# Optimization experiments

Measured on AMD Instinct MI355X. Metric: run time of the kernel, lower is better.

The kernel has to match this reference:

```python
import jax, jax.numpy as jnp
import numpy as np

N, E = 50000, 800000
IN_CH, HID, OUT, EDIM = 151, 128, 51, 51


def setup_inputs() -> dict:
    key = jax.random.key(0)
    ks = jax.random.split(key, 10)
    def w(k, shape, fan_in):
        return jax.random.normal(k, shape, jnp.float32) * (1.0 / np.sqrt(fan_in))
    return {
        "x": jax.random.normal(ks[0], (N, IN_CH), jnp.float32),
        "edge_attr": jax.random.normal(ks[1], (E, EDIM), jnp.float32),
        "W_edge0": w(ks[2], (EDIM, IN_CH), EDIM),
        "b_edge0": jnp.zeros((IN_CH,), jnp.float32),
        "W0": w(ks[3], (IN_CH, HID), IN_CH),
        "b0": jnp.zeros((HID,), jnp.float32),
        "W_edge1": w(ks[4], (EDIM, HID), EDIM),
        "b_edge1": jnp.zeros((HID,), jnp.float32),
        "W1": w(ks[5], (HID, HID), HID),
        "b1": jnp.zeros((HID,), jnp.float32),
        "W_out": w(ks[6], (HID, OUT), HID),
        "b_out": jnp.zeros((OUT,), jnp.float32),
        "edge_index": jax.random.randint(ks[7], (2, E), 0, N, jnp.int32),
    }


def gtn_layer(x, src, dst, edge_attr, W_e, b_e, W, b):
    # message: x_j + Linear(edge_attr);  aggr='add' scatter to dst.
    eat = edge_attr @ W_e + b_e                                # [E, in_ch]
    msgs = x[src] + eat                                        # gather + add
    agg = jax.ops.segment_sum(msgs, dst, num_segments=x.shape[0])
    # self-loops carry zero edge_attr -> transformed attr == bias b_e,
    # so their message is x + b_e (equivalent to concatenating N self-loop edges).
    agg = agg + x + b_e
    return agg @ W + b                                         # self.linear


def reference(x, edge_attr, W_edge0, b_edge0, W0, b0, W_edge1, b_edge1, W1, b1, W_out, b_out, edge_index):
    src, dst = edge_index[0], edge_index[1]
    h = gtn_layer(x, src, dst, edge_attr, W_edge0, b_edge0, W0, b0)   # [N, HID]
    h = gtn_layer(h, src, dst, edge_attr, W_edge1, b_edge1, W1, b1)   # [N, HID]
    # global_mean_pool with batch=arange(N) is identity (one node per graph)
    return h @ W_out + b_out                                          # [N, OUT]
```

## Files before the change

### kernel.cpp

```cpp
#include <hip/hip_runtime.h>

#define N_NODES 50000
#define N_EDGES 800000
#define IN_CH   151
#define HID     128
#define OUT_CH  51
#define EDIM    51
#define WP      64
#define LSTR    68
#define NBLK    ((N_NODES + 255) / 256)

static __device__ __forceinline__ unsigned int f2bf(float f) {
    union { float f; unsigned int u; } v; v.f = f;
    unsigned int r = v.u + 0x7FFF + ((v.u >> 16) & 1);
    return r >> 16;
}
static __device__ __forceinline__ float bflo(unsigned int u) {
    return __uint_as_float(u << 16);
}
static __device__ __forceinline__ float bfhi(unsigned int u) {
    return __uint_as_float(u & 0xFFFF0000u);
}

__global__ void kw1(const float* __restrict__ We0, const float* __restrict__ W0,
                    const float* __restrict__ be0, const float* __restrict__ W1,
                    const float* __restrict__ Wout,
                    float* __restrict__ M0, float* __restrict__ c0, float* __restrict__ Wc) {
    int t = blockIdx.x * blockDim.x + threadIdx.x;
    if (t < 51 * 128) {
        int i = t / 128, j = t % 128;
        float a = 0.f;
        for (int k = 0; k < IN_CH; ++k) a += We0[i * IN_CH + k] * W0[k * HID + j];
        M0[t] = a;
    } else if (t < 51 * 128 + 128) {
        int j = t - 51 * 128;
        float a = 0.f;
        for (int k = 0; k < IN_CH; ++k) a += be0[k] * W0[k * HID + j];
        c0[j] = a;
    } else if (t < 51 * 128 + 128 + 128 * WP) {
        int u = t - (51 * 128 + 128);
        int i = u / WP, j = u % WP;
        float a = 0.f;
        if (j < OUT_CH)
            for (int k = 0; k < HID; ++k) a += W1[i * HID + k] * Wout[k * OUT_CH + j];
        Wc[i * WP + j] = a;
    }
}

__global__ void kw2(const float* __restrict__ We1, const float* __restrict__ be1,
                    const float* __restrict__ b1, const float* __restrict__ Wout,
                    const float* __restrict__ bout, const float* __restrict__ Wc,
                    float* __restrict__ Mc, float* __restrict__ cc, float* __restrict__ dd) {
    int t = blockIdx.x * blockDim.x + threadIdx.x;
    if (t < 51 * WP) {
        int i = t / WP, j = t % WP;
        float a = 0.f;
        if (j < OUT_CH)
            for (int k = 0; k < HID; ++k) a += We1[i * HID + k] * Wc[k * WP + j];
        Mc[t] = a;
    } else if (t < 51 * WP + 51) {
        int j = t - 51 * WP;
        float a = 0.f;
        for (int k = 0; k < HID; ++k) a += be1[k] * Wc[k * WP + j];
        cc[j] = a;
    } else if (t < 51 * WP + 102) {
        int j = t - (51 * WP + 51);
        float a = 0.f;
        for (int k = 0; k < HID; ++k) a += b1[k] * Wout[k * OUT_CH + j];
        dd[j] = a + bout[j];
    }
}

__global__ void k_hist(const int* __restrict__ ei, int* __restrict__ deg) {
    int e = blockIdx.x * 256 + threadIdx.x;
    if (e >= N_EDGES) return;
    atomicAdd(&deg[ei[N_EDGES + e]], 1);
}

__global__ void scan1(const int* __restrict__ deg, int* __restrict__ blksum) {
    __shared__ int lds[256];
    int i = blockIdx.x * 256 + threadIdx.x;
    lds[threadIdx.x] = (i < N_NODES) ? deg[i] : 0;
    __syncthreads();
    for (int s = 128; s > 0; s >>= 1) {
        if (threadIdx.x < s) lds[threadIdx.x] += lds[threadIdx.x + s];
        __syncthreads();
    }
    if (threadIdx.x == 0) blksum[blockIdx.x] = lds[0];
}

__global__ void scan2(const int* __restrict__ blksum, int* __restrict__ blkoff) {
    __shared__ int lds[256];
    int v = (threadIdx.x < NBLK) ? blksum[threadIdx.x] : 0;
    lds[threadIdx.x] = v;
    __syncthreads();
    for (int s = 1; s < 256; s <<= 1) {
        int t = (threadIdx.x >= s) ? lds[threadIdx.x - s] : 0;
        __syncthreads();
        lds[threadIdx.x] += t;
        __syncthreads();
    }
    if (threadIdx.x < NBLK) blkoff[threadIdx.x] = lds[threadIdx.x] - v;
}

__global__ void scan3(const int* __restrict__ deg, const int* __restrict__ blkoff,
                      int* __restrict__ row_start, int* __restrict__ cursor) {
    __shared__ int lds[256];
    int i = blockIdx.x * 256 + threadIdx.x;
    int v = (i < N_NODES) ? deg[i] : 0;
    lds[threadIdx.x] = v;
    __syncthreads();
    for (int s = 1; s < 256; s <<= 1) {
        int t = (threadIdx.x >= s) ? lds[threadIdx.x - s] : 0;
        __syncthreads();
        lds[threadIdx.x] += t;
        __syncthreads();
    }
    if (i < N_NODES) {
        int ex = blkoff[blockIdx.x] + lds[threadIdx.x] - v;
        row_start[i] = ex;
        cursor[i] = ex;
    }
    if (blockIdx.x == 0 && threadIdx.x == 0) row_start[N_NODES] = N_EDGES;
}

__global__ void k_fill(const int* __restrict__ ei, int* __restrict__ cursor,
                       int* __restrict__ eid_sorted, int* __restrict__ src_sorted) {
    int e = blockIdx.x * 256 + threadIdx.x;
    if (e >= N_EDGES) return;
    int dst = ei[N_EDGES + e];
    int pos = atomicAdd(&cursor[dst], 1);
    eid_sorted[pos] = e;
    src_sorted[pos] = ei[e];
}

__global__ void k_agg_S(const float* __restrict__ ea, const int* __restrict__ eid_sorted,
                        const int* __restrict__ row_start, float* __restrict__ S) {
    int n = blockIdx.x * 4 + (threadIdx.x >> 6);
    if (n >= N_NODES) return;
    int lane = threadIdx.x & 63;
    int n0 = row_start[n], n1 = row_start[n + 1];
    float acc = 0.f;
    bool act = lane < EDIM;
    for (int base = n0; base < n1; base += 64) {
        int cnt = min(64, n1 - base);
        int eid_l = (base + lane < n1) ? eid_sorted[base + lane] : 0;
        int t = 0;
        for (; t + 8 <= cnt; t += 8) {
            int e0 = __shfl(eid_l, t),     e1 = __shfl(eid_l, t + 1);
            int e2 = __shfl(eid_l, t + 2), e3 = __shfl(eid_l, t + 3);
            int e4 = __shfl(eid_l, t + 4), e5 = __shfl(eid_l, t + 5);
            int e6 = __shfl(eid_l, t + 6), e7 = __shfl(eid_l, t + 7);
            float v0 = act ? ea[(size_t)e0 * EDIM + lane] : 0.f;
            float v1 = act ? ea[(size_t)e1 * EDIM + lane] : 0.f;
            float v2 = act ? ea[(size_t)e2 * EDIM + lane] : 0.f;
            float v3 = act ? ea[(size_t)e3 * EDIM + lane] : 0.f;
            float v4 = act ? ea[(size_t)e4 * EDIM + lane] : 0.f;
            float v5 = act ? ea[(size_t)e5 * EDIM + lane] : 0.f;
            float v6 = act ? ea[(size_t)e6 * EDIM + lane] : 0.f;
            float v7 = act ? ea[(size_t)e7 * EDIM + lane] : 0.f;
            acc += ((v0 + v1) + (v2 + v3)) + ((v4 + v5) + (v6 + v7));
        }
        for (; t < cnt; ++t) {
            int e0 = __shfl(eid_l, t);
            if (act) acc += ea[(size_t)e0 * EDIM + lane];
        }
    }
    if (act) S[(size_t)n * EDIM + lane] = acc;
}

__global__ void k_agg_h(const unsigned int* __restrict__ yb, const int* __restrict__ src_sorted,
                        const int* __restrict__ row_start, float* __restrict__ hacc) {
    int n = blockIdx.x * 4 + (threadIdx.x >> 6);
    if (n >= N_NODES) return;
    int lane = threadIdx.x & 63;
    int n0 = row_start[n], n1 = row_start[n + 1];
    float2 acc = make_float2(0.f, 0.f);
    for (int base = n0; base < n1; base += 64) {
        int cnt = min(64, n1 - base);
        int s_l = (base + lane < n1) ? src_sorted[base + lane] : 0;
        int t = 0;
        for (; t + 8 <= cnt; t += 8) {
            int s0 = __shfl(s_l, t),     s1 = __shfl(s_l, t + 1);
            int s2 = __shfl(s_l, t + 2), s3 = __shfl(s_l, t + 3);
            int s4 = __shfl(s_l, t + 4), s5 = __shfl(s_l, t + 5);
            int s6 = __shfl(s_l, t + 6), s7 = __shfl(s_l, t + 7);
            unsigned int v0 = yb[(size_t)s0 * 64 + lane];
            unsigned int v1 = yb[(size_t)s1 * 64 + lane];
            unsigned int v2 = yb[(size_t)s2 * 64 + lane];
            unsigned int v3 = yb[(size_t)s3 * 64 + lane];
            unsigned int v4 = yb[(size_t)s4 * 64 + lane];
            unsigned int v5 = yb[(size_t)s5 * 64 + lane];
            unsigned int v6 = yb[(size_t)s6 * 64 + lane];
            unsigned int v7 = yb[(size_t)s7 * 64 + lane];
            acc.x += ((bflo(v0) + bflo(v1)) + (bflo(v2) + bflo(v3)))
                   + ((bflo(v4) + bflo(v5)) + (bflo(v6) + bflo(v7)));
            acc.y += ((bfhi(v0) + bfhi(v1)) + (bfhi(v2) + bfhi(v3)))
                   + ((bfhi(v4) + bfhi(v5)) + (bfhi(v6) + bfhi(v7)));
        }
        for (; t < cnt; ++t) {
            int s0 = __shfl(s_l, t);
            unsigned int v0 = yb[(size_t)s0 * 64 + lane];
            acc.x += bflo(v0); acc.y += bfhi(v0);
        }
    }
    float2* hp = (float2*)(hacc + (size_t)n * HID) + lane;
    float2 old = *hp;
    old.x += acc.x; old.y += acc.y;
    *hp = old;
}

__global__ void k_agg_out(const unsigned short* __restrict__ wb, const int* __restrict__ src_sorted,
                          const int* __restrict__ row_start, float* __restrict__ out) {
    int n = blockIdx.x * 4 + (threadIdx.x >> 6);
    if (n >= N_NODES) return;
    int lane = threadIdx.x & 63;
    int n0 = row_start[n], n1 = row_start[n + 1];
    float acc = 0.f;
    bool act = lane < OUT_CH;
    for (int base = n0; base < n1; base += 64) {
        int cnt = min(64, n1 - base);
        int s_l = (base + lane < n1) ? src_sorted[base + lane] : 0;
        int t = 0;
        for (; t + 8 <= cnt; t += 8) {
            int s0 = __shfl(s_l, t),     s1 = __shfl(s_l, t + 1);
            int s2 = __shfl(s_l, t + 2), s3 = __shfl(s_l, t + 3);
            int s4 = __shfl(s_l, t + 4), s5 = __shfl(s_l, t + 5);
            int s6 = __shfl(s_l, t + 6), s7 = __shfl(s_l, t + 7);
            unsigned int v0 = act ? wb[(size_t)s0 * WP + lane] : 0u;
            unsigned int v1 = act ? wb[(size_t)s1 * WP + lane] : 0u;
            unsigned int v2 = act ? wb[(size_t)s2 * WP + lane] : 0u;
            unsigned int v3 = act ? wb[(size_t)s3 * WP + lane] : 0u;
            unsigned int v4 = act ? wb[(size_t)s4 * WP + lane] : 0u;
            unsigned int v5 = act ? wb[(size_t)s5 * WP + lane] : 0u;
            unsigned int v6 = act ? wb[(size_t)s6 * WP + lane] : 0u;
            unsigned int v7 = act ? wb[(size_t)s7 * WP + lane] : 0u;
            acc += ((bflo(v0) + bflo(v1)) + (bflo(v2) + bflo(v3)))
                 + ((bflo(v4) + bflo(v5)) + (bflo(v6) + bflo(v7)));
        }
        for (; t < cnt; ++t) {
            int s0 = __shfl(s_l, t);
            if (act) acc += bflo((unsigned int)wb[(size_t)s0 * WP + lane]);
        }
    }
    if (act) out[(size_t)n * OUT_CH + lane] += acc;
}

__global__ __launch_bounds__(256, 4) void k_layer0(
        const float* __restrict__ x, const float* __restrict__ W0,
        const float* __restrict__ b0, const float* __restrict__ S,
        const int* __restrict__ deg, const float* __restrict__ M0,
        const float* __restrict__ c0,
        unsigned int* __restrict__ yb, float* __restrict__ hacc) {
    __shared__ float aT[64 * LSTR];
    int tid = threadIdx.x;
    int r_base = blockIdx.x * 64;
    int cg = tid & 15, rg = tid >> 4;
    int c = cg * 8, r0 = rg * 4;

    float4 accA[4], accB[4];
#pragma unroll
    for (int i = 0; i < 4; ++i) {
        accA[i] = make_float4(0.f, 0.f, 0.f, 0.f);
        accB[i] = make_float4(0.f, 0.f, 0.f, 0.f);
    }

    for (int p = 0; p < 3; ++p) {
        int koff = p * 64;
        int chunk = min(64, IN_CH - koff);
        __syncthreads();
        for (int idx = tid; idx < 64 * 64; idx += 256) {
            int r = idx >> 6, kk = idx & 63;
            if (kk >= chunk) continue;
            int row = r_base + r;
            aT[kk * LSTR + r] = (row < N_NODES) ? x[(size_t)row * IN_CH + koff + kk] : 0.f;
        }
        __syncthreads();
#pragma unroll 4
        for (int kk = 0; kk < chunk; ++kk) {
            int k = koff + kk;
            float4 wv0 = *(const float4*)(W0 + k * HID + c);
            float4 wv1 = *(const float4*)(W0 + k * HID + c + 4);
            float4 a0 = *(const float4*)(&aT[kk * LSTR + r0]);
            float ar[4] = {a0.x, a0.y, a0.z, a0.w};
#pragma unroll
            for (int i = 0; i < 4; ++i) {
                accA[i].x += ar[i] * wv0.x; accA[i].y += ar[i] * wv0.y;
                accA[i].z += ar[i] * wv0.z; accA[i].w += ar[i] * wv0.w;
                accB[i].x += ar[i] * wv1.x; accB[i].y += ar[i] * wv1.y;
                accB[i].z += ar[i] * wv1.z; accB[i].w += ar[i] * wv1.w;
            }
        }
    }

#pragma unroll
    for (int i = 0; i < 4; ++i) {
        int row = r_base + r0 + i;
        if (row < N_NODES) {
            uint4 pk;
            pk.x = f2bf(accA[i].x) | (f2bf(accA[i].y) << 16);
            pk.y = f2bf(accA[i].z) | (f2bf(accA[i].w) << 16);
            pk.z = f2bf(accB[i].x) | (f2bf(accB[i].y) << 16);
            pk.w = f2bf(accB[i].z) | (f2bf(accB[i].w) << 16);
            *(uint4*)(yb + (size_t)row * 64 + (c >> 1)) = pk;
        }
    }

    __syncthreads();
    for (int idx = tid; idx < 64 * 64; idx += 256) {
        int r = idx >> 6, kk = idx & 63;
        if (kk >= EDIM) continue;
        int row = r_base + r;
        aT[kk * LSTR + r] = (row < N_NODES) ? S[(size_t)row * EDIM + kk] : 0.f;
    }
    __syncthreads();
#pragma unroll 4
    for (int kk = 0; kk < EDIM; ++kk) {
        float4 wv0 = *(const float4*)(M0 + kk * HID + c);
        float4 wv1 = *(const float4*)(M0 + kk * HID + c + 4);
        float4 a0 = *(const float4*)(&aT[kk * LSTR + r0]);
        float ar[4] = {a0.x, a0.y, a0.z, a0.w};
#pragma unroll
        for (int i = 0; i < 4; ++i) {
            accA[i].x += ar[i] * wv0.x; accA[i].y += ar[i] * wv0.y;
            accA[i].z += ar[i] * wv0.z; accA[i].w += ar[i] * wv0.w;
            accB[i].x += ar[i] * wv1.x; accB[i].y += ar[i] * wv1.y;
            accB[i].z += ar[i] * wv1.z; accB[i].w += ar[i] * wv1.w;
        }
    }

    float4 cv0 = *(const float4*)(c0 + c);
    float4 cv1 = *(const float4*)(c0 + c + 4);
    float4 bv0 = *(const float4*)(b0 + c);
    float4 bv1 = *(const float4*)(b0 + c + 4);
#pragma unroll
    for (int i = 0; i < 4; ++i) {
        int row = r_base + r0 + i;
        if (row < N_NODES) {
            float d1 = (float)(deg[row] + 1);
            float4 vA = accA[i], vB = accB[i];
            vA.x += d1 * cv0.x + bv0.x; vA.y += d1 * cv0.y + bv0.y;
            vA.z += d1 * cv0.z + bv0.z; vA.w += d1 * cv0.w + bv0.w;
            vB.x += d1 * cv1.x + bv1.x; vB.y += d1 * cv1.y + bv1.y;
            vB.z += d1 * cv1.z + bv1.z; vB.w += d1 * cv1.w + bv1.w;
            *(float4*)(hacc + (size_t)row * HID + c) = vA;
            *(float4*)(hacc + (size_t)row * HID + c + 4) = vB;
        }
    }
}

__global__ __launch_bounds__(256, 4) void k_layer1(
        const float* __restrict__ hacc, const float* __restrict__ Wc,
        const float* __restrict__ S, const int* __restrict__ deg,
        const float* __restrict__ Mc, const float* __restrict__ cc,
        const float* __restrict__ dd,
        unsigned int* __restrict__ wb, float* __restrict__ out) {
    __shared__ float aT[64 * LSTR];
    int tid = threadIdx.x;
    int r_base = blockIdx.x * 64;
    int cg = tid & 15, rg = tid >> 4;
    int c = cg * 4, r0 = rg * 4;

    float4 acc[4];
#pragma unroll
    for (int i = 0; i < 4; ++i) acc[i] = make_float4(0.f, 0.f, 0.f, 0.f);

    for (int p = 0; p < 2; ++p) {
        int koff = p * 64;
        __syncthreads();
        for (int idx = tid; idx < 64 * 64; idx += 256) {
            int r = idx >> 6, kk = idx & 63;
            int row = r_base + r;
            aT[kk * LSTR + r] = (row < N_NODES) ? hacc[(size_t)row * HID + koff + kk] : 0.f;
        }
        __syncthreads();
#pragma unroll 4
        for (int kk = 0; kk < 64; ++kk) {
            int k = koff + kk;
            float4 wv = *(const float4*)(Wc + k * WP + c);
            float4 a0 = *(const float4*)(&aT[kk * LSTR + r0]);
            float ar[4] = {a0.x, a0.y, a0.z, a0.w};
#pragma unroll
            for (int i = 0; i < 4; ++i) {
                acc[i].x += ar[i] * wv.x; acc[i].y += ar[i] * wv.y;
                acc[i].z += ar[i] * wv.z; acc[i].w += ar[i] * wv.w;
            }
        }
    }

#pragma unroll
    for (int i = 0; i < 4; ++i) {
        int row = r_base + r0 + i;
        if (row < N_NODES) {
            uint2 pk;
            pk.x = f2bf(acc[i].x) | (f2bf(acc[i].y) << 16);
            pk.y = f2bf(acc[i].z) | (f2bf(acc[i].w) << 16);
            *(uint2*)(wb + (size_t)row * 32 + (c >> 1)) = pk;
        }
    }

    __syncthreads();
    for (int idx = tid; idx < 64 * 64; idx += 256) {
        int r = idx >> 6, kk = idx & 63;
        if (kk >= EDIM) continue;
        int row = r_base + r;
        aT[kk * LSTR + r] = (row < N_NODES) ? S[(size_t)row * EDIM + kk] : 0.f;
    }
    __syncthreads();
#pragma unroll 4
    for (int kk = 0; kk < EDIM; ++kk) {
        float4 wv = *(const float4*)(Mc + kk * WP + c);
        float4 a0 = *(const float4*)(&aT[kk * LSTR + r0]);
        float ar[4] = {a0.x, a0.y, a0.z, a0.w};
#pragma unroll
        for (int i = 0; i < 4; ++i) {
            acc[i].x += ar[i] * wv.x; acc[i].y += ar[i] * wv.y;
            acc[i].z += ar[i] * wv.z; acc[i].w += ar[i] * wv.w;
        }
    }

    if (c < OUT_CH) {
        float cv[4], dv[4];
#pragma unroll
        for (int j = 0; j < 4; ++j) {
            int col = c + j;
            cv[j] = (col < OUT_CH) ? cc[col] : 0.f;
            dv[j] = (col < OUT_CH) ? dd[col] : 0.f;
        }
#pragma unroll
        for (int i = 0; i < 4; ++i) {
            int row = r_base + r0 + i;
            if (row < N_NODES) {
                float d1 = (float)(deg[row] + 1);
                const float* ap = (const float*)&acc[i];
#pragma unroll
                for (int j = 0; j < 4; ++j) {
                    int col = c + j;
                    if (col < OUT_CH)
                        out[(size_t)row * OUT_CH + col] = ap[j] + d1 * cv[j] + dv[j];
                }
            }
        }
    }
}

extern "C" void kernel_launch(void* const* d_in, const int* in_sizes, int n_in,
                              void* d_out, int out_size, void* d_ws, size_t ws_size,
                              hipStream_t stream) {
    const float* x    = (const float*)d_in[0];
    const float* ea   = (const float*)d_in[1];
    const float* We0  = (const float*)d_in[2];
    const float* be0  = (const float*)d_in[3];
    const float* W0   = (const float*)d_in[4];
    const float* b0   = (const float*)d_in[5];
    const float* We1  = (const float*)d_in[6];
    const float* be1  = (const float*)d_in[7];
    const float* W1   = (const float*)d_in[8];
    const float* b1   = (const float*)d_in[9];
    const float* Wout = (const float*)d_in[10];
    const float* bout = (const float*)d_in[11];
    const int*   ei   = (const int*)d_in[12];
    float* out = (float*)d_out;

    char* p = (char*)d_ws;
    auto alloc = [&](size_t bytes) {
        char* r = p;
        p += (bytes + 255) & ~(size_t)255;
        return r;
    };
    float* S         = (float*)alloc((size_t)N_NODES * EDIM * 4);
    int*   deg       = (int*)  alloc((size_t)N_NODES * 4);
    int*   row_start = (int*)  alloc((size_t)(N_NODES + 1) * 4);
    int*   cursor    = (int*)  alloc((size_t)N_NODES * 4);
    int*   blksum    = (int*)  alloc((size_t)NBLK * 4);
    int*   blkoff    = (int*)  alloc((size_t)NBLK * 4);
    int*   eid_srt   = (int*)  alloc((size_t)N_EDGES * 4);
    int*   src_srt   = (int*)  alloc((size_t)N_EDGES * 4);
    unsigned int* yb = (unsigned int*)alloc((size_t)N_NODES * 64 * 4);
    float* hacc      = (float*)alloc((size_t)N_NODES * HID * 4);
    unsigned int* wb = (unsigned int*)alloc((size_t)N_NODES * 32 * 4);
    float* M0        = (float*)alloc(51 * 128 * 4);
    float* c0        = (float*)alloc(128 * 4);
    float* Wc        = (float*)alloc(128 * WP * 4);
    float* Mc        = (float*)alloc(51 * WP * 4);
    float* cc        = (float*)alloc(51 * 4);
    float* dd        = (float*)alloc(51 * 4);

    hipMemsetAsync(deg, 0, (size_t)N_NODES * 4, stream);

    kw1<<<(51 * 128 + 128 + 128 * WP + 255) / 256, 256, 0, stream>>>(
        We0, W0, be0, W1, Wout, M0, c0, Wc);
    kw2<<<(51 * WP + 102 + 255) / 256, 256, 0, stream>>>(
        We1, be1, b1, Wout, bout, Wc, Mc, cc, dd);

    k_hist<<<(N_EDGES + 255) / 256, 256, 0, stream>>>(ei, deg);
    scan1<<<NBLK, 256, 0, stream>>>(deg, blksum);
    scan2<<<1, 256, 0, stream>>>(blksum, blkoff);
    scan3<<<NBLK, 256, 0, stream>>>(deg, blkoff, row_start, cursor);
    k_fill<<<(N_EDGES + 255) / 256, 256, 0, stream>>>(ei, cursor, eid_srt, src_srt);

    k_agg_S<<<(N_NODES + 3) / 4, 256, 0, stream>>>(ea, eid_srt, row_start, S);

    k_layer0<<<(N_NODES + 63) / 64, 256, 0, stream>>>(x, W0, b0, S, deg, M0, c0, yb, hacc);
    k_agg_h<<<(N_NODES + 3) / 4, 256, 0, stream>>>(yb, src_srt, row_start, hacc);

    k_layer1<<<(N_NODES + 63) / 64, 256, 0, stream>>>(hacc, Wc, S, deg, Mc, cc, dd, wb, out);
    k_agg_out<<<(N_NODES + 3) / 4, 256, 0, stream>>>((const unsigned short*)wb, src_srt, row_start, out);
}
```

Baseline: 613.8 us.

## Split node aggregation across two waves, pack edge arrays, shrink GEMM row tiles

Each node's edge list is now split between two wavefronts that interleave 64-edge chunks and combine partial sums through shared memory, doubling parallelism per node in all three gather kernels. The separate sorted edge-id and source arrays are merged into one int2 array written by a single store in the fill kernel. The dense layer kernels drop from 64 to 32 rows per block with 2 rows per thread and a smaller LDS tile, trading register reuse for more blocks and occupancy. The risks are added block-level syncs, 8-byte strided reads when only one field is needed, and less arithmetic reuse in the GEMMs.

```diff
diff --git a/kernel.cpp b/kernel.cpp
--- a/kernel.cpp
+++ b/kernel.cpp
@@ -7,7 +7,7 @@
 #define OUT_CH  51
 #define EDIM    51
 #define WP      64
-#define LSTR    68
+#define L0STR   34
 #define NBLK    ((N_NODES + 255) / 256)
 
 static __device__ __forceinline__ unsigned int f2bf(float f) {
@@ -125,26 +125,30 @@
 }
 
 __global__ void k_fill(const int* __restrict__ ei, int* __restrict__ cursor,
-                       int* __restrict__ eid_sorted, int* __restrict__ src_sorted) {
+                       int2* __restrict__ es) {
     int e = blockIdx.x * 256 + threadIdx.x;
     if (e >= N_EDGES) return;
-    int dst = ei[N_EDGES + e];
+    int src = ei[e], dst = ei[N_EDGES + e];
     int pos = atomicAdd(&cursor[dst], 1);
-    eid_sorted[pos] = e;
-    src_sorted[pos] = ei[e];
-}
-
-__global__ void k_agg_S(const float* __restrict__ ea, const int* __restrict__ eid_sorted,
+    es[pos] = make_int2(e, src);
+}
+
+
+__global__ void k_agg_S(const float* __restrict__ ea, const int2* __restrict__ es,
                         const int* __restrict__ row_start, float* __restrict__ S) {
-    int n = blockIdx.x * 4 + (threadIdx.x >> 6);
-    if (n >= N_NODES) return;
-    int lane = threadIdx.x & 63;
-    int n0 = row_start[n], n1 = row_start[n + 1];
+    __shared__ float cmb[2][2][64];
+    int tid = threadIdx.x;
+    int wv = tid >> 6, lane = tid & 63;
+    int pair = wv >> 1, h = wv & 1;
+    int n = blockIdx.x * 2 + pair;
+    bool valid = n < N_NODES;
+    int n0 = 0, n1 = 0;
+    if (valid) { n0 = row_start[n]; n1 = row_start[n + 1]; }
     float acc = 0.f;
     bool act = lane < EDIM;
-    for (int base = n0; base < n1; base += 64) {
+    for (int base = n0 + h * 64; base < n1; base += 128) {
         int cnt = min(64, n1 - base);
-        int eid_l = (base + lane < n1) ? eid_sorted[base + lane] : 0;
+        int eid_l = (base + lane < n1) ? es[base + lane].x : 0;
         int t = 0;
         for (; t + 8 <= cnt; t += 8) {
             int e0 = __shfl(eid_l, t),     e1 = __shfl(eid_l, t + 1);
@@ -166,19 +170,26 @@
             if (act) acc += ea[(size_t)e0 * EDIM + lane];
         }
     }
-    if (act) S[(size_t)n * EDIM + lane] = acc;
-}
-
-__global__ void k_agg_h(const unsigned int* __restrict__ yb, const int* __restrict__ src_sorted,
+    cmb[pair][h][lane] = acc;
+    __syncthreads();
+    if (h == 0 && valid && act)
+        S[(size_t)n * EDIM + lane] = cmb[pair][0][lane] + cmb[pair][1][lane];
+}
+
+__global__ void k_agg_h(const unsigned int* __restrict__ yb, const int2* __restrict__ es,
                         const int* __restrict__ row_start, float* __restrict__ hacc) {
-    int n = blockIdx.x * 4 + (threadIdx.x >> 6);
-    if (n >= N_NODES) return;
-    int lane = threadIdx.x & 63;
-    int n0 = row_start[n], n1 = row_start[n + 1];
+    __shared__ float cmb[2][2][128];
+    int tid = threadIdx.x;
+    int wv = tid >> 6, lane = tid & 63;
+    int pair = wv >> 1, h = wv & 1;
+    int n = blockIdx.x * 2 + pair;
+    bool valid = n < N_NODES;
+    int n0 = 0, n1 = 0;
+    if (valid) { n0 = row_start[n]; n1 = row_start[n + 1]; }
     float2 acc = make_float2(0.f, 0.f);
-    for (int base = n0; base < n1; base += 64) {
+    for (int base = n0 + h * 64; base < n1; base += 128) {
         int cnt = min(64, n1 - base);
-        int s_l = (base + lane < n1) ? src_sorted[base + lane] : 0;
+        int s_l = (base + lane < n1) ? es[base + lane].y : 0;
         int t = 0;
         for (; t + 8 <= cnt; t += 8) {
             int s0 = __shfl(s_l, t),     s1 = __shfl(s_l, t + 1);
@@ -204,23 +215,33 @@
             acc.x += bflo(v0); acc.y += bfhi(v0);
         }
     }
-    float2* hp = (float2*)(hacc + (size_t)n * HID) + lane;
-    float2 old = *hp;
-    old.x += acc.x; old.y += acc.y;
-    *hp = old;
-}
-
-__global__ void k_agg_out(const unsigned short* __restrict__ wb, const int* __restrict__ src_sorted,
+    cmb[pair][h][lane * 2]     = acc.x;
+    cmb[pair][h][lane * 2 + 1] = acc.y;
+    __syncthreads();
+    if (h == 0 && valid) {
+        float2* hp = (float2*)(hacc + (size_t)n * HID) + lane;
+        float2 old = *hp;
+        old.x += cmb[pair][0][lane * 2]     + cmb[pair][1][lane * 2];
+        old.y += cmb[pair][0][lane * 2 + 1] + cmb[pair][1][lane * 2 + 1];
+        *hp = old;
+    }
+}
+
+__global__ void k_agg_out(const unsigned short* __restrict__ wb, const int2* __restrict__ es,
                           const int* __restrict__ row_start, float* __restrict__ out) {
-    int n = blockIdx.x * 4 + (threadIdx.x >> 6);
-    if (n >= N_NODES) return;
-    int lane = threadIdx.x & 63;
-    int n0 = row_start[n], n1 = row_start[n + 1];
+    __shared__ float cmb[2][2][64];
+    int tid = threadIdx.x;
+    int wv = tid >> 6, lane = tid & 63;
+    int pair = wv >> 1, h = wv & 1;
+    int n = blockIdx.x * 2 + pair;
+    bool valid = n < N_NODES;
+    int n0 = 0, n1 = 0;
+    if (valid) { n0 = row_start[n]; n1 = row_start[n + 1]; }
     float acc = 0.f;
     bool act = lane < OUT_CH;
-    for (int base = n0; base < n1; base += 64) {
+    for (int base = n0 + h * 64; base < n1; base += 128) {
         int cnt = min(64, n1 - base);
-        int s_l = (base + lane < n1) ? src_sorted[base + lane] : 0;
+        int s_l = (base + lane < n1) ? es[base + lane].y : 0;
         int t = 0;
         for (; t + 8 <= cnt; t += 8) {
             int s0 = __shfl(s_l, t),     s1 = __shfl(s_l, t + 1);
@@ -243,102 +264,103 @@
             if (act) acc += bflo((unsigned int)wb[(size_t)s0 * WP + lane]);
         }
     }
-    if (act) out[(size_t)n * OUT_CH + lane] += acc;
-}
-
-__global__ __launch_bounds__(256, 4) void k_layer0(
+    cmb[pair][h][lane] = acc;
+    __syncthreads();
+    if (h == 0 && valid && act)
+        out[(size_t)n * OUT_CH + lane] += cmb[pair][0][lane] + cmb[pair][1][lane];
+}
+
+__global__ __launch_bounds__(256) void k_layer0(
         const float* __restrict__ x, const float* __restrict__ W0,
         const float* __restrict__ b0, const float* __restrict__ S,
         const int* __restrict__ deg, const float* __restrict__ M0,
         const float* __restrict__ c0,
         unsigned int* __restrict__ yb, float* __restrict__ hacc) {
-    __shared__ float aT[64 * LSTR];
+    __shared__ float aT[64 * L0STR];
     int tid = threadIdx.x;
-    int r_base = blockIdx.x * 64;
+    int r_base = blockIdx.x * 32;
     int cg = tid & 15, rg = tid >> 4;
-    int c = cg * 8, r0 = rg * 4;
-
-    float4 accA[4], accB[4];
-#pragma unroll
-    for (int i = 0; i < 4; ++i) {
-        accA[i] = make_float4(0.f, 0.f, 0.f, 0.f);
-        accB[i] = make_float4(0.f, 0.f, 0.f, 0.f);
-    }
+    int c = cg * 8, r0 = rg * 2;
+
+    float4 a0A = make_float4(0.f, 0.f, 0.f, 0.f), a0B = a0A;
+    float4 a1A = a0A, a1B = a0A;
 
     for (int p = 0; p < 3; ++p) {
         int koff = p * 64;
         int chunk = min(64, IN_CH - koff);
         __syncthreads();
-        for (int idx = tid; idx < 64 * 64; idx += 256) {
+#pragma unroll
+        for (int idx = tid; idx < 32 * 64; idx += 256) {
             int r = idx >> 6, kk = idx & 63;
-            if (kk >= chunk) continue;
             int row = r_base + r;
-            aT[kk * LSTR + r] = (row < N_NODES) ? x[(size_t)row * IN_CH + koff + kk] : 0.f;
+            float v = 0.f;
+            if (kk < chunk && row < N_NODES) v = x[(size_t)row * IN_CH + koff + kk];
+            aT[kk * L0STR + r] = v;
         }
         __syncthreads();
 #pragma unroll 4
         for (int kk = 0; kk < chunk; ++kk) {
             int k = koff + kk;
-            float4 wv0 = *(const float4*)(W0 + k * HID + c);
-            float4 wv1 = *(const float4*)(W0 + k * HID + c + 4);
-            float4 a0 = *(const float4*)(&aT[kk * LSTR + r0]);
-            float ar[4] = {a0.x, a0.y, a0.z, a0.w};
-#pragma unroll
-            for (int i = 0; i < 4; ++i) {
-                accA[i].x += ar[i] * wv0.x; accA[i].y += ar[i] * wv0.y;
-                accA[i].z += ar[i] * wv0.z; accA[i].w += ar[i] * wv0.w;
-                accB[i].x += ar[i] * wv1.x; accB[i].y += ar[i] * wv1.y;
-                accB[i].z += ar[i] * wv1.z; accB[i].w += ar[i] * wv1.w;
-            }
-        }
-    }
-
-#pragma unroll
-    for (int i = 0; i < 4; ++i) {
-        int row = r_base + r0 + i;
+            float4 w0 = *(const float4*)(W0 + k * HID + c);
+            float4 w1 = *(const float4*)(W0 + k * HID + c + 4);
+            float2 a = *(const float2*)(&aT[kk * L0STR + r0]);
+            a0A.x += a.x * w0.x; a0A.y += a.x * w0.y; a0A.z += a.x * w0.z; a0A.w += a.x * w0.w;
+            a0B.x += a.x * w1.x; a0B.y += a.x * w1.y; a0B.z += a.x * w1.z; a0B.w += a.x * w1.w;
+            a1A.x += a.y * w0.x; a1A.y += a.y * w0.y; a1A.z += a.y * w0.z; a1A.w += a.y * w0.w;
+            a1B.x += a.y * w1.x; a1B.y += a.y * w1.y; a1B.z += a.y * w1.z; a1B.w += a.y * w1.w;
+        }
+    }
+
+    {
+        int row = r_base + r0;
         if (row < N_NODES) {
             uint4 pk;
-            pk.x = f2bf(accA[i].x) | (f2bf(accA[i].y) << 16);
-            pk.y = f2bf(accA[i].z) | (f2bf(accA[i].w) << 16);
-            pk.z = f2bf(accB[i].x) | (f2bf(accB[i].y) << 16);
-            pk.w = f2bf(accB[i].z) | (f2bf(accB[i].w) << 16);
+            pk.x = f2bf(a0A.x) | (f2bf(a0A.y) << 16);
+            pk.y = f2bf(a0A.z) | (f2bf(a0A.w) << 16);
+            pk.z = f2bf(a0B.x) | (f2bf(a0B.y) << 16);
+            pk.w = f2bf(a0B.z) | (f2bf(a0B.w) << 16);
             *(uint4*)(yb + (size_t)row * 64 + (c >> 1)) = pk;
         }
-    }
-
-    __syncthreads();
-    for (int idx = tid; idx < 64 * 64; idx += 256) {
+        if (row + 1 < N_NODES) {
+            uint4 pk;
+            pk.x = f2bf(a1A.x) | (f2bf(a1A.y) << 16);
+            pk.y = f2bf(a1A.z) | (f2bf(a1A.w) << 16);
+            pk.z = f2bf(a1B.x) | (f2bf(a1B.y) << 16);
+            pk.w = f2bf(a1B.z) | (f2bf(a1B.w) << 16);
+            *(uint4*)(yb + (size_t)(row + 1) * 64 + (c >> 1)) = pk;
+        }
+    }
+
+    __syncthreads();
+#pragma unroll
+    for (int idx = tid; idx < 32 * 64; idx += 256) {
         int r = idx >> 6, kk = idx & 63;
-        if (kk >= EDIM) continue;
         int row = r_base + r;
-        aT[kk * LSTR + r] = (row < N_NODES) ? S[(size_t)row * EDIM + kk] : 0.f;
+        float v = 0.f;
+        if (kk < EDIM && row < N_NODES) v = S[(size_t)row * EDIM + kk];
+        aT[kk * L0STR + r] = v;
     }
     __syncthreads();
 #pragma unroll 4
     for (int kk = 0; kk < EDIM; ++kk) {
-        float4 wv0 = *(const float4*)(M0 + kk * HID + c);
-        float4 wv1 = *(const float4*)(M0 + kk * HID + c + 4);
-        float4 a0 = *(const float4*)(&aT[kk * LSTR + r0]);
-        float ar[4] = {a0.x, a0.y, a0.z, a0.w};
-#pragma unroll
-        for (int i = 0; i < 4; ++i) {
-            accA[i].x += ar[i] * wv0.x; accA[i].y += ar[i] * wv0.y;
-            accA[i].z += ar[i] * wv0.z; accA[i].w += ar[i] * wv0.w;
-            accB[i].x += ar[i] * wv1.x; accB[i].y += ar[i] * wv1.y;
-            accB[i].z += ar[i] * wv1.z; accB[i].w += ar[i] * wv1.w;
-        }
+        float4 w0 = *(const float4*)(M0 + kk * HID + c);
+        float4 w1 = *(const float4*)(M0 + kk * HID + c + 4);
+        float2 a = *(const float2*)(&aT[kk * L0STR + r0]);
+        a0A.x += a.x * w0.x; a0A.y += a.x * w0.y; a0A.z += a.x * w0.z; a0A.w += a.x * w0.w;
+        a0B.x += a.x * w1.x; a0B.y += a.x * w1.y; a0B.z += a.x * w1.z; a0B.w += a.x * w1.w;
+        a1A.x += a.y * w0.x; a1A.y += a.y * w0.y; a1A.z += a.y * w0.z; a1A.w += a.y * w0.w;
+        a1B.x += a.y * w1.x; a1B.y += a.y * w1.y; a1B.z += a.y * w1.z; a1B.w += a.y * w1.w;
     }
 
     float4 cv0 = *(const float4*)(c0 + c);
     float4 cv1 = *(const float4*)(c0 + c + 4);
     float4 bv0 = *(const float4*)(b0 + c);
     float4 bv1 = *(const float4*)(b0 + c + 4);
-#pragma unroll
-    for (int i = 0; i < 4; ++i) {
-        int row = r_base + r0 + i;
+    {
+        int row = r_base + r0;
         if (row < N_NODES) {
             float d1 = (float)(deg[row] + 1);
-            float4 vA = accA[i], vB = accB[i];
+            float4 vA = a0A, vB = a0B;
             vA.x += d1 * cv0.x + bv0.x; vA.y += d1 * cv0.y + bv0.y;
             vA.z += d1 * cv0.z + bv0.z; vA.w += d1 * cv0.w + bv0.w;
             vB.x += d1 * cv1.x + bv1.x; vB.y += d1 * cv1.y + bv1.y;
@@ -346,77 +368,85 @@
             *(float4*)(hacc + (size_t)row * HID + c) = vA;
             *(float4*)(hacc + (size_t)row * HID + c + 4) = vB;
         }
-    }
-}
-
-__global__ __launch_bounds__(256, 4) void k_layer1(
+        if (row + 1 < N_NODES) {
+            float d1 = (float)(deg[row + 1] + 1);
+            float4 vA = a1A, vB = a1B;
+            vA.x += d1 * cv0.x + bv0.x; vA.y += d1 * cv0.y + bv0.y;
+            vA.z += d1 * cv0.z + bv0.z; vA.w += d1 * cv0.w + bv0.w;
+            vB.x += d1 * cv1.x + bv1.x; vB.y += d1 * cv1.y + bv1.y;
+            vB.z += d1 * cv1.z + bv1.z; vB.w += d1 * cv1.w + bv1.w;
+            *(float4*)(hacc + (size_t)(row + 1) * HID + c) = vA;
+            *(float4*)(hacc + (size_t)(row + 1) * HID + c + 4) = vB;
+        }
+    }
+}
+
+__global__ __launch_bounds__(256) void k_layer1(
         const float* __restrict__ hacc, const float* __restrict__ Wc,
         const float* __restrict__ S, const int* __restrict__ deg,
         const float* __restrict__ Mc, const float* __restrict__ cc,
         const float* __restrict__ dd,
         unsigned int* __restrict__ wb, float* __restrict__ out) {
-    __shared__ float aT[64 * LSTR];
+    __shared__ float aT[64 * L0STR];
     int tid = threadIdx.x;
-    int r_base = blockIdx.x * 64;
+    int r_base = blockIdx.x * 32;
     int cg = tid & 15, rg = tid >> 4;
-    int c = cg * 4, r0 = rg * 4;
-
-    float4 acc[4];
-#pragma unroll
-    for (int i = 0; i < 4; ++i) acc[i] = make_float4(0.f, 0.f, 0.f, 0.f);
+    int c = cg * 4, r0 = rg * 2;
+
+    float4 acc0 = make_float4(0.f, 0.f, 0.f, 0.f), acc1 = acc0;
 
     for (int p = 0; p < 2; ++p) {
         int koff = p * 64;
         __syncthreads();
-        for (int idx = tid; idx < 64 * 64; idx += 256) {
+#pragma unroll
+        for (int idx = tid; idx < 32 * 64; idx += 256) {
             int r = idx >> 6, kk = idx & 63;
             int row = r_base + r;
-            aT[kk * LSTR + r] = (row < N_NODES) ? hacc[(size_t)row * HID + koff + kk] : 0.f;
+            aT[kk * L0STR + r] = (row < N_NODES) ? hacc[(size_t)row * HID + koff + kk] : 0.f;
         }
         __syncthreads();
 #pragma unroll 4
         for (int kk = 0; kk < 64; ++kk) {
             int k = koff + kk;
             float4 wv = *(const float4*)(Wc + k * WP + c);
-            float4 a0 = *(const float4*)(&aT[kk * LSTR + r0]);
-            float ar[4] = {a0.x, a0.y, a0.z, a0.w};
-#pragma unroll
-            for (int i = 0; i < 4; ++i) {
-                acc[i].x += ar[i] * wv.x; acc[i].y += ar[i] * wv.y;
-                acc[i].z += ar[i] * wv.z; acc[i].w += ar[i] * wv.w;
-            }
-        }
-    }
-
-#pragma unroll
-    for (int i = 0; i < 4; ++i) {
-        int row = r_base + r0 + i;
+            float2 a = *(const float2*)(&aT[kk * L0STR + r0]);
+            acc0.x += a.x * wv.x; acc0.y += a.x * wv.y; acc0.z += a.x * wv.z; acc0.w += a.x * wv.w;
+            acc1.x += a.y * wv.x; acc1.y += a.y * wv.y; acc1.z += a.y * wv.z; acc1.w += a.y * wv.w;
+        }
+    }
+
+    {
+        int row = r_base + r0;
         if (row < N_NODES) {
             uint2 pk;
-            pk.x = f2bf(acc[i].x) | (f2bf(acc[i].y) << 16);
-            pk.y = f2bf(acc[i].z) | (f2bf(acc[i].w) << 16);
+            pk.x = f2bf(acc0.x) | (f2bf(acc0.y) << 16);
+            pk.y = f2bf(acc0.z) | (f2bf(acc0.w) << 16);
             *(uint2*)(wb + (size_t)row * 32 + (c >> 1)) = pk;
         }
-    }
-
-    __syncthreads();
-    for (int idx = tid; idx < 64 * 64; idx += 256) {
+        if (row + 1 < N_NODES) {
+            uint2 pk;
+            pk.x = f2bf(acc1.x) | (f2bf(acc1.y) << 16);
+            pk.y = f2bf(acc1.z) | (f2bf(acc1.w) << 16);
+            *(uint2*)(wb + (size_t)(row + 1) * 32 + (c >> 1)) = pk;
+        }
+    }
+
+    __syncthreads();
+#pragma unroll
+    for (int idx = tid; idx < 32 * 64; idx += 256) {
         int r = idx >> 6, kk = idx & 63;
-        if (kk >= EDIM) continue;
         int row = r_base + r;
-        aT[kk * LSTR + r] = (row < N_NODES) ? S[(size_t)row * EDIM + kk] : 0.f;
+        float v = 0.f;
+        if (kk < EDIM && row < N_NODES) v = S[(size_t)row * EDIM + kk];
+        aT[kk * L0STR + r] = v;
     }
     __syncthreads();
 #pragma unroll 4
     for (int kk = 0; kk < EDIM; ++kk) {
         float4 wv = *(const float4*)(Mc + kk * WP + c);
-        float4 a0 = *(const float4*)(&aT[kk * LSTR + r0]);
-        float ar[4] = {a0.x, a0.y, a0.z, a0.w};
-#pragma unroll
-        for (int i = 0; i < 4; ++i) {
-            acc[i].x += ar[i] * wv.x; acc[i].y += ar[i] * wv.y;
-            acc[i].z += ar[i] * wv.z; acc[i].w += ar[i] * wv.w;
-        }
+        float2 a = *(const float2*)(&aT[kk * L0STR + r0]);
+        acc0.x += a.x * wv.x; acc0.y += a.x * wv.y; acc0.z += a.x * wv.z; acc0.w += a.x * wv.w;
+        acc1.x += a.y * wv.x; acc1.y += a.y * wv.y; acc1.z += a.y * wv.z; acc1.w += a.y * wv.w;
     }
 
     if (c < OUT_CH) {
@@ -427,18 +457,25 @@
             cv[j] = (col < OUT_CH) ? cc[col] : 0.f;
             dv[j] = (col < OUT_CH) ? dd[col] : 0.f;
         }
-#pragma unroll
-        for (int i = 0; i < 4; ++i) {
-            int row = r_base + r0 + i;
-            if (row < N_NODES) {
-                float d1 = (float)(deg[row] + 1);
-                const float* ap = (const float*)&acc[i];
-#pragma unroll
-                for (int j = 0; j < 4; ++j) {
-                    int col = c + j;
-                    if (col < OUT_CH)
-                        out[(size_t)row * OUT_CH + col] = ap[j] + d1 * cv[j] + dv[j];
-                }
+        int row = r_base + r0;
+        if (row < N_NODES) {
+            float d1 = (float)(deg[row] + 1);
+            const float* ap = (const float*)&acc0;
+#pragma unroll
+            for (int j = 0; j < 4; ++j) {
+                int col = c + j;
+                if (col < OUT_CH)
+                    out[(size_t)row * OUT_CH + col] = ap[j] + d1 * cv[j] + dv[j];
+            }
+        }
+        if (row + 1 < N_NODES) {
+            float d1 = (float)(deg[row + 1] + 1);
+            const float* ap = (const float*)&acc1;
+#pragma unroll
+            for (int j = 0; j < 4; ++j) {
+                int col = c + j;
+                if (col < OUT_CH)
+                    out[(size_t)(row + 1) * OUT_CH + col] = ap[j] + d1 * cv[j] + dv[j];
             }
         }
     }
@@ -474,8 +511,7 @@
     int*   cursor    = (int*)  alloc((size_t)N_NODES * 4);
     int*   blksum    = (int*)  alloc((size_t)NBLK * 4);
     int*   blkoff    = (int*)  alloc((size_t)NBLK * 4);
-    int*   eid_srt   = (int*)  alloc((size_t)N_EDGES * 4);
-    int*   src_srt   = (int*)  alloc((size_t)N_EDGES * 4);
+    int2*  es        = (int2*) alloc((size_t)N_EDGES * 8);
     unsigned int* yb = (unsigned int*)alloc((size_t)N_NODES * 64 * 4);
     float* hacc      = (float*)alloc((size_t)N_NODES * HID * 4);
     unsigned int* wb = (unsigned int*)alloc((size_t)N_NODES * 32 * 4);
@@ -497,13 +533,13 @@
     scan1<<<NBLK, 256, 0, stream>>>(deg, blksum);
     scan2<<<1, 256, 0, stream>>>(blksum, blkoff);
     scan3<<<NBLK, 256, 0, stream>>>(deg, blkoff, row_start, cursor);
-    k_fill<<<(N_EDGES + 255) / 256, 256, 0, stream>>>(ei, cursor, eid_srt, src_srt);
-
-    k_agg_S<<<(N_NODES + 3) / 4, 256, 0, stream>>>(ea, eid_srt, row_start, S);
-
-    k_layer0<<<(N_NODES + 63) / 64, 256, 0, stream>>>(x, W0, b0, S, deg, M0, c0, yb, hacc);
-    k_agg_h<<<(N_NODES + 3) / 4, 256, 0, stream>>>(yb, src_srt, row_start, hacc);
-
-    k_layer1<<<(N_NODES + 63) / 64, 256, 0, stream>>>(hacc, Wc, S, deg, Mc, cc, dd, wb, out);
-    k_agg_out<<<(N_NODES + 3) / 4, 256, 0, stream>>>((const unsigned short*)wb, src_srt, row_start, out);
-}
+    k_fill<<<(N_EDGES + 255) / 256, 256, 0, stream>>>(ei, cursor, es);
+
+    k_agg_S<<<(N_NODES + 1) / 2, 256, 0, stream>>>(ea, es, row_start, S);
+
+    k_layer0<<<(N_NODES + 31) / 32, 256, 0, stream>>>(x, W0, b0, S, deg, M0, c0, yb, hacc);
+    k_agg_h<<<(N_NODES + 1) / 2, 256, 0, stream>>>(yb, es, row_start, hacc);
+
+    k_layer1<<<(N_NODES + 31) / 32, 256, 0, stream>>>(hacc, Wc, S, deg, Mc, cc, dd, wb, out);
+    k_agg_out<<<(N_NODES + 1) / 2, 256, 0, stream>>>((const unsigned short*)wb, es, row_start, out);
+}
```

After: 716.9 us. 16.8% more time.
